# Kernel tuning notes

Measured on AMD Instinct MI355X. Metric: run time of the kernel, lower is better.

Reference implementation:

```python
import jax, jax.numpy as jnp
import numpy as np

KEY_BITS = 1024
VALUE_BITS = 1024
CAPACITY = 65536
BATCH = 2048


def setup_inputs() -> dict:
    key = jax.random.key(0)
    kq, kk, kv = jax.random.split(key, 3)
    query = jax.random.randint(kq, (BATCH, KEY_BITS), 0, 2, dtype=jnp.int32)
    keys = jax.random.randint(kk, (CAPACITY, KEY_BITS), 0, 2, dtype=jnp.int32)
    values = jax.random.normal(kv, (CAPACITY, VALUE_BITS), dtype=jnp.float32)
    return {"query": query, "keys": keys, "values": values}


def reference(query, keys, values):
    # Hamming mismatches between 0/1 bit vectors via GEMM:
    #   popcount(q ^ k) = sum(q) + sum(k) - 2 * (q . k)
    qf = query.astype(jnp.float32)                      # [B, key_bits]
    kf = keys.astype(jnp.float32)                       # [C, key_bits]
    dot = jnp.einsum('bk,ck->bc', qf, kf)               # [B, C]
    mismatches = qf.sum(axis=1, keepdims=True) + kf.sum(axis=1)[None, :] - 2.0 * dot
    sim = KEY_BITS - mismatches                         # similarity = key_bits - Hamming dist
    best_idx = jnp.argmax(sim, axis=1)                  # first max, matches strict '>' loop
    return values[best_idx]                             # [B, value_bits]
```

## Files before the change

### kernel.cpp

```cpp
#include <hip/hip_runtime.h>
#include <stdint.h>

typedef int v4i  __attribute__((ext_vector_type(4)));
typedef int v16i __attribute__((ext_vector_type(16)));

#define CAPACITY  65536
#define BATCH     2048
#define KBITS     1024
#define NSTEP     16


__global__ void prep_qT_kernel(const int* __restrict__ in,
                               uint32_t* __restrict__ outT) {
    const int row = blockIdx.x, t = threadIdx.x;
    int4 v = reinterpret_cast<const int4*>(in)[(size_t)row * 256 + t];
    uint32_t b = (uint32_t)(v.x & 1)        | ((uint32_t)(v.y & 1) << 8) |
                 ((uint32_t)(v.z & 1) << 16) | ((uint32_t)(v.w & 1) << 24);
    outT[(size_t)(t >> 2) * (BATCH * 4) + (size_t)row * 4 + (t & 3)] = b;
}

__global__ void prep_i8_kernel(const int* __restrict__ in,
                               unsigned char* __restrict__ out8,
                               int* __restrict__ sums) {
    const int row = blockIdx.x, t = threadIdx.x;
    int4 v = reinterpret_cast<const int4*>(in)[(size_t)row * 256 + t];
    uint32_t b = (uint32_t)(v.x & 1)        | ((uint32_t)(v.y & 1) << 8) |
                 ((uint32_t)(v.z & 1) << 16) | ((uint32_t)(v.w & 1) << 24);
    reinterpret_cast<uint32_t*>(out8)[(size_t)row * 256 + t] = b;
    int s = (v.x & 1) + (v.y & 1) + (v.z & 1) + (v.w & 1);
    for (int off = 32; off; off >>= 1) s += __shfl_xor(s, off, 64);
    __shared__ int ws4[4];
    if ((t & 63) == 0) ws4[t >> 6] = s;
    __syncthreads();
    if (t == 0) sums[row] = ws4[0] + ws4[1] + ws4[2] + ws4[3];
}

__global__ void init_best_kernel(uint32_t* __restrict__ best) {
    best[blockIdx.x * 256 + threadIdx.x] = 0xFFFFFFFFu;
}

__device__ __forceinline__ int swz(int idx) { return idx ^ ((idx >> 3) & 7); }

__launch_bounds__(256, 4)
__global__ void gemm_scan_kernel(const uint4* __restrict__ aT4,
                                 const unsigned char* __restrict__ ki8,
                                 const int* __restrict__ sumk,
                                 uint32_t* __restrict__ best) {
    __shared__ uint4 sB[3][256];

    const int t    = threadIdx.x;
    const int lane = t & 63, wid = t >> 6;
    const int ln   = lane & 31, kh = lane >> 5;

    const int b     = blockIdx.x;
    const int slot  = b >> 3;
    const int ntile = (b & 7) * 128 + (slot >> 3);
    const int mtile = slot & 7;
    const int m0 = mtile * 256, n0 = ntile * 64;

    const int sidx = swz(t);
    const unsigned char* bSrc =
        ki8 + (size_t)(n0 + (sidx >> 2)) * KBITS + (sidx & 3) * 16;
    auto STAGE_B = [&](int buf, int kc) {
        __builtin_amdgcn_global_load_lds(
            (const __attribute__((address_space(1))) void*)(bSrc + kc),
            (__attribute__((address_space(3))) void*)&sB[buf][wid * 64],
            16, 0, 0);
    };

    int offB[2][2];
#pragma unroll
    for (int km = 0; km < 2; ++km)
#pragma unroll
        for (int ct = 0; ct < 2; ++ct)
            offB[km][ct] = swz((ct * 32 + ln) * 4 + km * 2 + kh);

    const int mbase = m0 + wid * 64 + ln;

    v16i acc[2][2];
#pragma unroll
    for (int rt = 0; rt < 2; ++rt)
#pragma unroll
        for (int ct = 0; ct < 2; ++ct)
#pragma unroll
            for (int e = 0; e < 16; ++e) acc[rt][ct][e] = 0;

    uint4 afbuf[2][2][2];
    auto LOAD_AF = [&](int par, int s) {
#pragma unroll
        for (int km = 0; km < 2; ++km)
#pragma unroll
            for (int rt = 0; rt < 2; ++rt)
                afbuf[par][km][rt] = aT4[(size_t)(s * 4 + km * 2 + kh) * BATCH
                                         + mbase + rt * 32];
    };

    STAGE_B(0, 0);
    STAGE_B(1, 64);
    LOAD_AF(0, 0);
    asm volatile("s_waitcnt vmcnt(5)" ::: "memory");
    __builtin_amdgcn_s_barrier();

#pragma unroll
    for (int s = 0; s < NSTEP; ++s) {
        const int par = s & 1, buf = s % 3;

        if (s + 1 < NSTEP) LOAD_AF(par ^ 1, s + 1);
        if (s + 2 < NSTEP) STAGE_B((s + 2) % 3, (s + 2) * 64);

        uint4 bf0[2], bf1[2];
#pragma unroll
        for (int ct = 0; ct < 2; ++ct) bf0[ct] = sB[buf][offB[0][ct]];
#pragma unroll
        for (int ct = 0; ct < 2; ++ct) bf1[ct] = sB[buf][offB[1][ct]];

        if (s == 0)
            asm volatile("s_waitcnt vmcnt(5) lgkmcnt(2)" ::: "memory");
        else if (s <= 13)
            asm volatile("s_waitcnt vmcnt(6) lgkmcnt(2)" ::: "memory");
        else if (s == 14)
            asm volatile("s_waitcnt vmcnt(5) lgkmcnt(2)" ::: "memory");
        else
            asm volatile("s_waitcnt vmcnt(0) lgkmcnt(2)" ::: "memory");
        __builtin_amdgcn_sched_barrier(0);

        __builtin_amdgcn_s_setprio(1);
#pragma unroll
        for (int rt = 0; rt < 2; ++rt)
#pragma unroll
            for (int ct = 0; ct < 2; ++ct)
                acc[rt][ct] = __builtin_amdgcn_mfma_i32_32x32x32_i8(
                    *(v4i*)&afbuf[par][0][rt], *(v4i*)&bf0[ct], acc[rt][ct], 0, 0, 0);
        __builtin_amdgcn_s_setprio(0);

        asm volatile("s_waitcnt lgkmcnt(0)" ::: "memory");
        __builtin_amdgcn_sched_barrier(0);

        __builtin_amdgcn_s_setprio(1);
#pragma unroll
        for (int rt = 0; rt < 2; ++rt)
#pragma unroll
            for (int ct = 0; ct < 2; ++ct)
                acc[rt][ct] = __builtin_amdgcn_mfma_i32_32x32x32_i8(
                    *(v4i*)&afbuf[par][1][rt], *(v4i*)&bf1[ct], acc[rt][ct], 0, 0, 0);
        __builtin_amdgcn_s_setprio(0);

        if (s < NSTEP - 1) {
            if (s <= 13)
                asm volatile("s_waitcnt vmcnt(5)" ::: "memory");
            else
                asm volatile("s_waitcnt vmcnt(4)" ::: "memory");
            __builtin_amdgcn_s_barrier();
        }
    }

    int sk[2];
#pragma unroll
    for (int ct = 0; ct < 2; ++ct) sk[ct] = sumk[n0 + ct * 32 + ln];

#pragma unroll
    for (int rt = 0; rt < 2; ++rt) {
#pragma unroll
        for (int r = 0; r < 16; ++r) {
            const int qrow = m0 + wid * 64 + rt * 32 + (r & 3) + 8 * (r >> 2) + 4 * kh;
            uint32_t bmin = 0xFFFFFFFFu;
#pragma unroll
            for (int ct = 0; ct < 2; ++ct) {
                uint32_t dist = (uint32_t)(sk[ct] - 2 * acc[rt][ct][r] + 2048);
                uint32_t col  = (uint32_t)(n0 + ct * 32 + ln);
                bmin = min(bmin, (dist << 16) | col);
            }
#pragma unroll
            for (int off = 1; off < 32; off <<= 1)
                bmin = min(bmin, (uint32_t)__shfl_xor((int)bmin, off, 64));
            if (ln == 0) atomicMin(&best[qrow], bmin);
        }
    }
}

__global__ void finalize_kernel(const uint32_t* __restrict__ best,
                                const float* __restrict__ values,
                                float* __restrict__ out) {
    const int qy  = blockIdx.x;
    const int idx = (int)(best[qy] & 0xFFFFu);
    const float4* v4 = reinterpret_cast<const float4*>(values) + (size_t)idx * 256;
    float4* o4 = reinterpret_cast<float4*>(out) + (size_t)qy * 256;
    o4[threadIdx.x] = v4[threadIdx.x];
}

#define KCHUNK 256
#define NSPLIT (CAPACITY / KCHUNK)

__device__ __forceinline__ uint32_t pack_word(const int4* __restrict__ p) {
    uint32_t word = 0;
#pragma unroll
    for (int j = 0; j < 8; ++j) {
        int4 v = p[j];
        word |= (uint32_t)(v.x & 1) << (4 * j + 0);
        word |= (uint32_t)(v.y & 1) << (4 * j + 1);
        word |= (uint32_t)(v.z & 1) << (4 * j + 2);
        word |= (uint32_t)(v.w & 1) << (4 * j + 3);
    }
    return word;
}

__global__ void pack_bits_kernel(const int* __restrict__ in,
                                 uint32_t* __restrict__ out, int nwords) {
    int w = blockIdx.x * blockDim.x + threadIdx.x;
    if (w >= nwords) return;
    out[w] = pack_word(reinterpret_cast<const int4*>(in) + (size_t)w * 8);
}

__launch_bounds__(256, 4)
__global__ void scan_kernel(const uint32_t* __restrict__ qpack,
                            const uint32_t* __restrict__ kpack,
                            uint32_t* __restrict__ best) {
    const int t      = threadIdx.x;
    const int lane   = t & 63;
    const int wid    = t >> 6;
    const int ksplit = blockIdx.x & (NSPLIT - 1);
    const int qgb    = blockIdx.x >> 8;
    const int query  = qgb * 256 + wid * 64 + lane;

    uint32_t q[32];
    const uint4* qp4 = reinterpret_cast<const uint4*>(qpack + (size_t)query * 32);
#pragma unroll
    for (int j = 0; j < 8; ++j) {
        uint4 v = qp4[j];
        q[4 * j + 0] = v.x; q[4 * j + 1] = v.y;
        q[4 * j + 2] = v.z; q[4 * j + 3] = v.w;
    }
    uint32_t bst = 0xFFFFFFFFu;
    const int k0 = ksplit * KCHUNK;
#pragma unroll 2
    for (int k = k0; k < k0 + KCHUNK; ++k) {
        const uint4* kw4 = reinterpret_cast<const uint4*>(kpack + (size_t)k * 32);
        uint32_t dist = 0;
#pragma unroll
        for (int j = 0; j < 8; ++j) {
            uint4 kv = kw4[j];
            dist += __popc(kv.x ^ q[4 * j + 0]);
            dist += __popc(kv.y ^ q[4 * j + 1]);
            dist += __popc(kv.z ^ q[4 * j + 2]);
            dist += __popc(kv.w ^ q[4 * j + 3]);
        }
        bst = min(bst, (dist << 16) | (uint32_t)k);
    }
    atomicMin(&best[query], bst);
}

extern "C" void kernel_launch(void* const* d_in, const int* in_sizes, int n_in,
                              void* d_out, int out_size, void* d_ws, size_t ws_size,
                              hipStream_t stream) {
    const int*   query  = (const int*)d_in[0];
    const int*   keys   = (const int*)d_in[1];
    const float* values = (const float*)d_in[2];
    float*       out    = (float*)d_out;
    char* ws = (char*)d_ws;

    const size_t need = 2097152ULL + 67108864ULL + 262144ULL + 8192ULL;
    if (ws_size >= need) {
        uint32_t* qT  = (uint32_t*)ws;
        unsigned char* ki8 = (unsigned char*)(ws + 2097152);
        int* sumk = (int*)(ws + 2097152 + 67108864);
        uint32_t* best = (uint32_t*)(ws + 2097152 + 67108864 + 262144);

        init_best_kernel<<<BATCH / 256, 256, 0, stream>>>(best);
        prep_qT_kernel<<<BATCH,    256, 0, stream>>>(query, qT);
        prep_i8_kernel<<<CAPACITY, 256, 0, stream>>>(keys, ki8, sumk);
        gemm_scan_kernel<<<8192, 256, 0, stream>>>(
            reinterpret_cast<const uint4*>(qT), ki8, sumk, best);
        finalize_kernel<<<BATCH, 256, 0, stream>>>(best, values, out);
    } else {
        uint32_t* qpack = (uint32_t*)ws;
        uint32_t* kpack = (uint32_t*)(ws + 262144);
        uint32_t* best  = (uint32_t*)(ws + 262144 + 8388608);

        init_best_kernel<<<BATCH / 256, 256, 0, stream>>>(best);
        pack_bits_kernel<<<BATCH * 32 / 256, 256, 0, stream>>>(query, qpack, BATCH * 32);
        pack_bits_kernel<<<CAPACITY * 32 / 256, 256, 0, stream>>>(keys, kpack, CAPACITY * 32);
        scan_kernel<<<8 * NSPLIT, 256, 0, stream>>>(qpack, kpack, best);
        finalize_kernel<<<BATCH, 256, 0, stream>>>(best, values, out);
    }
}
```

Measured before the change: 280.8 us.

## Double K-chunk per pipeline step with new LDS swizzle and split A prefetch

```diff
diff --git a/kernel.cpp b/kernel.cpp
--- a/kernel.cpp
+++ b/kernel.cpp
@@ -7,7 +7,7 @@
 #define CAPACITY  65536
 #define BATCH     2048
 #define KBITS     1024
-#define NSTEP     16
+#define NSTEP     8
 
 
 __global__ void prep_qT_kernel(const int* __restrict__ in,
@@ -39,14 +39,16 @@
     best[blockIdx.x * 256 + threadIdx.x] = 0xFFFFFFFFu;
 }
 
-__device__ __forceinline__ int swz(int idx) { return idx ^ ((idx >> 3) & 7); }
+__device__ __forceinline__ int swz2(int idx) {
+    return idx ^ (((idx >> 3) ^ (idx >> 6)) & 7);
+}
 
 __launch_bounds__(256, 4)
 __global__ void gemm_scan_kernel(const uint4* __restrict__ aT4,
                                  const unsigned char* __restrict__ ki8,
                                  const int* __restrict__ sumk,
                                  uint32_t* __restrict__ best) {
-    __shared__ uint4 sB[3][256];
+    __shared__ uint4 sB[3][512];
 
     const int t    = threadIdx.x;
     const int lane = t & 63, wid = t >> 6;
@@ -58,22 +60,24 @@
     const int mtile = slot & 7;
     const int m0 = mtile * 256, n0 = ntile * 64;
 
-    const int sidx = swz(t);
-    const unsigned char* bSrc =
-        ki8 + (size_t)(n0 + (sidx >> 2)) * KBITS + (sidx & 3) * 16;
+    const int s0 = swz2(t), s1 = swz2(256 + t);
+    const unsigned char* bSrc0 = ki8 + (size_t)(n0 + (s0 >> 3)) * KBITS + (s0 & 7) * 16;
+    const unsigned char* bSrc1 = ki8 + (size_t)(n0 + (s1 >> 3)) * KBITS + (s1 & 7) * 16;
     auto STAGE_B = [&](int buf, int kc) {
         __builtin_amdgcn_global_load_lds(
-            (const __attribute__((address_space(1))) void*)(bSrc + kc),
-            (__attribute__((address_space(3))) void*)&sB[buf][wid * 64],
-            16, 0, 0);
+            (const __attribute__((address_space(1))) void*)(bSrc0 + kc),
+            (__attribute__((address_space(3))) void*)&sB[buf][t], 16, 0, 0);
+        __builtin_amdgcn_global_load_lds(
+            (const __attribute__((address_space(1))) void*)(bSrc1 + kc),
+            (__attribute__((address_space(3))) void*)&sB[buf][256 + t], 16, 0, 0);
     };
 
-    int offB[2][2];
-#pragma unroll
-    for (int km = 0; km < 2; ++km)
+    int offB[4][2];
+#pragma unroll
+    for (int km = 0; km < 4; ++km)
 #pragma unroll
         for (int ct = 0; ct < 2; ++ct)
-            offB[km][ct] = swz((ct * 32 + ln) * 4 + km * 2 + kh);
+            offB[km][ct] = swz2((ct * 32 + ln) * 8 + km * 2 + kh);
 
     const int mbase = m0 + wid * 64 + ln;
 
@@ -85,43 +89,46 @@
 #pragma unroll
             for (int e = 0; e < 16; ++e) acc[rt][ct][e] = 0;
 
-    uint4 afbuf[2][2][2];
-    auto LOAD_AF = [&](int par, int s) {
+    uint4 af01[2][2], af23[2][2];
+    auto LOAD_AF01 = [&](int s) {
 #pragma unroll
         for (int km = 0; km < 2; ++km)
 #pragma unroll
             for (int rt = 0; rt < 2; ++rt)
-                afbuf[par][km][rt] = aT4[(size_t)(s * 4 + km * 2 + kh) * BATCH
-                                         + mbase + rt * 32];
+                af01[km][rt] = aT4[(size_t)(s * 8 + km * 2 + kh) * BATCH
+                                   + mbase + rt * 32];
     };
+    auto LOAD_AF23 = [&](int s) {
+#pragma unroll
+        for (int km = 0; km < 2; ++km)
+#pragma unroll
+            for (int rt = 0; rt < 2; ++rt)
+                af23[km][rt] = aT4[(size_t)(s * 8 + 4 + km * 2 + kh) * BATCH
+                                   + mbase + rt * 32];
+    };
 
     STAGE_B(0, 0);
-    STAGE_B(1, 64);
-    LOAD_AF(0, 0);
-    asm volatile("s_waitcnt vmcnt(5)" ::: "memory");
+    LOAD_AF01(0);
+    STAGE_B(1, 128);
+    asm volatile("s_waitcnt vmcnt(6)" ::: "memory");
     __builtin_amdgcn_s_barrier();
 
 #pragma unroll
     for (int s = 0; s < NSTEP; ++s) {
-        const int par = s & 1, buf = s % 3;
-
-        if (s + 1 < NSTEP) LOAD_AF(par ^ 1, s + 1);
-        if (s + 2 < NSTEP) STAGE_B((s + 2) % 3, (s + 2) * 64);
-
-        uint4 bf0[2], bf1[2];
-#pragma unroll
-        for (int ct = 0; ct < 2; ++ct) bf0[ct] = sB[buf][offB[0][ct]];
-#pragma unroll
-        for (int ct = 0; ct < 2; ++ct) bf1[ct] = sB[buf][offB[1][ct]];
-
-        if (s == 0)
-            asm volatile("s_waitcnt vmcnt(5) lgkmcnt(2)" ::: "memory");
-        else if (s <= 13)
+        const int buf = s % 3;
+
+        LOAD_AF23(s);
+
+        uint4 bf[2][2];
+#pragma unroll
+        for (int ct = 0; ct < 2; ++ct) bf[0][ct] = sB[buf][offB[0][ct]];
+#pragma unroll
+        for (int ct = 0; ct < 2; ++ct) bf[1][ct] = sB[buf][offB[1][ct]];
+
+        if (s < NSTEP - 1)
             asm volatile("s_waitcnt vmcnt(6) lgkmcnt(2)" ::: "memory");
-        else if (s == 14)
-            asm volatile("s_waitcnt vmcnt(5) lgkmcnt(2)" ::: "memory");
         else
-            asm volatile("s_waitcnt vmcnt(0) lgkmcnt(2)" ::: "memory");
+            asm volatile("s_waitcnt vmcnt(4) lgkmcnt(2)" ::: "memory");
         __builtin_amdgcn_sched_barrier(0);
 
         __builtin_amdgcn_s_setprio(1);
@@ -130,7 +137,7 @@
 #pragma unroll
             for (int ct = 0; ct < 2; ++ct)
                 acc[rt][ct] = __builtin_amdgcn_mfma_i32_32x32x32_i8(
-                    *(v4i*)&afbuf[par][0][rt], *(v4i*)&bf0[ct], acc[rt][ct], 0, 0, 0);
+                    *(v4i*)&af01[0][rt], *(v4i*)&bf[0][ct], acc[rt][ct], 0, 0, 0);
         __builtin_amdgcn_s_setprio(0);
 
         asm volatile("s_waitcnt lgkmcnt(0)" ::: "memory");
@@ -142,16 +149,41 @@
 #pragma unroll
             for (int ct = 0; ct < 2; ++ct)
                 acc[rt][ct] = __builtin_amdgcn_mfma_i32_32x32x32_i8(
-                    *(v4i*)&afbuf[par][1][rt], *(v4i*)&bf1[ct], acc[rt][ct], 0, 0, 0);
+                    *(v4i*)&af01[1][rt], *(v4i*)&bf[1][ct], acc[rt][ct], 0, 0, 0);
         __builtin_amdgcn_s_setprio(0);
 
-        if (s < NSTEP - 1) {
-            if (s <= 13)
-                asm volatile("s_waitcnt vmcnt(5)" ::: "memory");
-            else
-                asm volatile("s_waitcnt vmcnt(4)" ::: "memory");
-            __builtin_amdgcn_s_barrier();
-        }
+#pragma unroll
+        for (int ct = 0; ct < 2; ++ct) bf[0][ct] = sB[buf][offB[2][ct]];
+#pragma unroll
+        for (int ct = 0; ct < 2; ++ct) bf[1][ct] = sB[buf][offB[3][ct]];
+
+        asm volatile("s_waitcnt vmcnt(0) lgkmcnt(2)" ::: "memory");
+        __builtin_amdgcn_sched_barrier(0);
+
+        __builtin_amdgcn_s_setprio(1);
+#pragma unroll
+        for (int rt = 0; rt < 2; ++rt)
+#pragma unroll
+            for (int ct = 0; ct < 2; ++ct)
+                acc[rt][ct] = __builtin_amdgcn_mfma_i32_32x32x32_i8(
+                    *(v4i*)&af23[0][rt], *(v4i*)&bf[0][ct], acc[rt][ct], 0, 0, 0);
+        __builtin_amdgcn_s_setprio(0);
+
+        asm volatile("s_waitcnt lgkmcnt(0)" ::: "memory");
+        __builtin_amdgcn_sched_barrier(0);
+
+        __builtin_amdgcn_s_setprio(1);
+#pragma unroll
+        for (int rt = 0; rt < 2; ++rt)
+#pragma unroll
+            for (int ct = 0; ct < 2; ++ct)
+                acc[rt][ct] = __builtin_amdgcn_mfma_i32_32x32x32_i8(
+                    *(v4i*)&af23[1][rt], *(v4i*)&bf[1][ct], acc[rt][ct], 0, 0, 0);
+        __builtin_amdgcn_s_setprio(0);
+
+        if (s + 1 < NSTEP) LOAD_AF01(s + 1);
+        if (s + 2 < NSTEP) STAGE_B((s + 2) % 3, (s + 2) * 128);
+        if (s < NSTEP - 1) __builtin_amdgcn_s_barrier();
     }
 
     int sk[2];
```

Result: slower. 335.8 us (+19.6%).
